# Optimization experiments

Hardware: AMD Instinct MI355X
Metric: run time of the kernel (lower is better)

## Reference

```python
import jax, jax.numpy as jnp
import numpy as np

N_NODES = 50000
N_EDGES = 800000
N_GRAPHS = 256
IN_DIM, HIDDEN_DIM, EMBED_DIM = 128, 64, 128


def setup_inputs() -> dict:
    key = jax.random.key(0)
    ks = jax.random.split(key, 8)
    x = jax.random.normal(ks[0], (N_NODES, IN_DIM), dtype=jnp.float32)
    edge_index = jax.random.randint(ks[1], (2, N_EDGES), 0, N_NODES, dtype=jnp.int64)
    edge_weight = jax.random.uniform(ks[2], (N_EDGES,), dtype=jnp.float32)
    batch_vec = jnp.sort(jax.random.randint(ks[3], (N_NODES,), 0, N_GRAPHS, dtype=jnp.int64))
    # Glorot-ish params for the two GCNConv layers
    W1 = jax.random.normal(ks[4], (IN_DIM, HIDDEN_DIM), dtype=jnp.float32) / np.sqrt(IN_DIM)
    b1 = jnp.zeros((HIDDEN_DIM,), dtype=jnp.float32)
    W2 = jax.random.normal(ks[5], (HIDDEN_DIM, EMBED_DIM), dtype=jnp.float32) / np.sqrt(HIDDEN_DIM)
    b2 = jnp.zeros((EMBED_DIM,), dtype=jnp.float32)
    return {"x": x, "edge_index": edge_index, "edge_weight": edge_weight,
            "batch_vec": batch_vec, "W1": W1, "b1": b1, "W2": W2, "b2": b2}


def _gcn_conv(x, src, dst, ew, W, b, num_nodes):
    # PyG GCNConv: linear transform, add self-loops (weight 1), sym-normalize, aggregate at dst.
    h = x @ W  # [N, out]
    loops = jnp.arange(num_nodes, dtype=src.dtype)
    row = jnp.concatenate([src, loops])
    col = jnp.concatenate([dst, loops])
    w = jnp.concatenate([ew, jnp.ones((num_nodes,), x.dtype)])
    deg = jax.ops.segment_sum(w, col, num_segments=num_nodes)
    dis = jnp.where(deg > 0, jax.lax.rsqrt(deg), 0.0)  # deg^{-1/2}, inf -> 0
    norm = dis[row] * w * dis[col]  # [E+N]
    msg = h[row] * norm[:, None]  # gather + scale
    out = jax.ops.segment_sum(msg, col, num_segments=num_nodes)  # scatter-add
    return out + b


def reference(x, edge_index, edge_weight, batch_vec, W1, b1, W2, b2):
    src, dst = edge_index[0], edge_index[1]
    h = jax.nn.relu(_gcn_conv(x, src, dst, edge_weight, W1, b1, N_NODES))
    # dropout is identity at inference
    h = jax.nn.relu(_gcn_conv(h, src, dst, edge_weight, W2, b2, N_NODES))
    # global_mean_pool over graphs
    s = jax.ops.segment_sum(h, batch_vec, num_segments=N_GRAPHS)
    cnt = jax.ops.segment_sum(jnp.ones((N_NODES,), h.dtype), batch_vec, num_segments=N_GRAPHS)
    return s / jnp.maximum(cnt, 1.0)[:, None]
```

## Files before the change

### kernel.cpp

```cpp
#include <hip/hip_runtime.h>

constexpr int N_NODES  = 50000;
constexpr int N_EDGES  = 800000;
constexpr int N_GRAPHS = 256;
constexpr int IN_DIM   = 128;
constexpr int HID      = 64;
constexpr int EMB      = 128;
constexpr int NBKT     = 391;
constexpr int BCAP     = 4096;
constexpr int EB       = (N_EDGES + 1023) / 1024;
constexpr int GB       = (N_NODES + 31) / 32;
constexpr int GSB      = (N_NODES + 255) / 256;
constexpr int NB2      = 64;

constexpr size_t OFF_POOL = 0;
constexpr size_t OFF_GCUR = 32768;
constexpr size_t OFF_GST  = 33160;
constexpr size_t OFF_DIS  = 33424;
constexpr size_t OFF_RS   = 83424;
constexpr size_t OFF_REC  = 133424;
constexpr size_t OFF_PART = OFF_REC + 2 * (size_t)NBKT * BCAP;
constexpr size_t OFF_H1   = OFF_PART;
constexpr size_t OFF_H1P  = OFF_PART + 4 * (size_t)NBKT * BCAP;
constexpr size_t OFF_AGG2 = OFF_H1P;

__device__ inline unsigned bf16r(float f) {
    unsigned u = __float_as_uint(f);
    return (u + 0x7fffu + ((u >> 16) & 1u)) >> 16;
}
__device__ inline unsigned bf16pack2(float lo, float hi) {
    return bf16r(lo) | (bf16r(hi) << 16);
}
__device__ inline float bflo(unsigned v) { return __uint_as_float(v << 16); }
__device__ inline float bfhi(unsigned v) { return __uint_as_float(v & 0xffff0000u); }

__device__ inline void fma4(float4& acc, float s, const float4& v) {
    acc.x += s * v.x; acc.y += s * v.y; acc.z += s * v.z; acc.w += s * v.w;
}

__global__ __launch_bounds__(256) void k_p2(const int* __restrict__ src,
                                            const int* __restrict__ dst,
                                            const float* __restrict__ ew,
                                            int* __restrict__ gcur,
                                            uint4* __restrict__ part,
                                            const int* __restrict__ batch,
                                            int* __restrict__ gstart) {
    __shared__ int   lb[NBKT];
    __shared__ int   lc[NBKT];
    __shared__ int   es[1024];
    __shared__ int   ed[1024];
    __shared__ float ee[1024];
    int tid = threadIdx.x;
    if (blockIdx.x >= EB) {
        int i = (blockIdx.x - EB) * 256 + tid;
        if (i >= N_NODES) return;
        int g = batch[i];
        if (i == 0) {
            for (int gg = 0; gg <= g; ++gg) gstart[gg] = 0;
        } else {
            int gp = batch[i - 1];
            for (int gg = gp + 1; gg <= g; ++gg) gstart[gg] = i;
        }
        if (i == N_NODES - 1) {
            for (int gg = g + 1; gg <= N_GRAPHS; ++gg) gstart[gg] = N_NODES;
        }
        return;
    }
    for (int i = tid; i < NBKT; i += 256) lc[i] = 0;
    __syncthreads();
    int base = blockIdx.x * 1024;
    #pragma unroll
    for (int j = 0; j < 4; ++j) {
        int idx = j * 256 + tid;
        int e = base + idx;
        int d = 0, s = 0; float w = 0.f;
        if (e < N_EDGES) {
            d = dst[e]; s = src[e]; w = ew[e];
            atomicAdd(&lc[d >> 7], 1);
        }
        es[idx] = s; ed[idx] = d; ee[idx] = w;
    }
    __syncthreads();
    for (int i = tid; i < NBKT; i += 256) {
        int c = lc[i];
        lb[i] = c ? (i * BCAP + atomicAdd(&gcur[i], c)) : 0;
        lc[i] = 0;
    }
    __syncthreads();
    #pragma unroll
    for (int j = 0; j < 4; ++j) {
        int idx = j * 256 + tid;
        int e = base + idx;
        if (e < N_EDGES) {
            int d = ed[idx];
            int b = d >> 7;
            int r = atomicAdd(&lc[b], 1);
            part[lb[b] + r] = make_uint4((unsigned)es[idx], (unsigned)d,
                                         __float_as_uint(ee[idx]), 0u);
        }
    }
}

constexpr int SMEM_BYTES = 32768 + 32 * (IN_DIM + 4) * 4;
__global__ __launch_bounds__(256) void k_p3_gemm1(const uint4* __restrict__ part,
                                                  const int* __restrict__ gcur,
                                                  int* __restrict__ rs,
                                                  float* __restrict__ dis,
                                                  uint2* __restrict__ rec,
                                                  const float* __restrict__ x,
                                                  const float* __restrict__ W1,
                                                  unsigned* __restrict__ h) {
    __shared__ alignas(16) unsigned char smem[SMEM_BYTES];
    int tid = threadIdx.x;
    if (blockIdx.x < NBKT) {
        uint2* cache = (uint2*)smem;
        int*   cnt   = (int*)(smem + 32768);
        float* dgw   = (float*)(smem + 32768 + 512);
        int*   scn   = (int*)(smem + 32768 + 1024);
        int*   curx  = (int*)(smem + 32768 + 1536);
        int b = blockIdx.x;
        int ebeg = b * BCAP;
        int ne = gcur[b]; if (ne > BCAP) ne = BCAP;
        if (tid < 128) { cnt[tid] = 0; dgw[tid] = 0.f; }
        __syncthreads();
        for (int i = tid; i < ne; i += 256) {
            uint4 r = part[ebeg + i];
            int ld = (int)r.y & 127;
            cache[i] = make_uint2(r.x | ((unsigned)ld << 16), r.z);
            atomicAdd(&cnt[ld], 1);
            atomicAdd(&dgw[ld], __uint_as_float(r.z));
        }
        __syncthreads();
        int c  = (tid < 128) ? cnt[tid] : 0;
        int pc = (c + 1) & ~1;
        if (tid < 128) scn[tid] = pc;
        __syncthreads();
        for (int off = 1; off < 128; off <<= 1) {
            int a = (tid >= off && tid < 128) ? scn[tid - off] : 0;
            __syncthreads();
            if (tid < 128) scn[tid] += a;
            __syncthreads();
        }
        if (tid < 128) {
            int start = ebeg + scn[tid] - pc;
            int node = (b << 7) + tid;
            if (node < N_NODES) {
                rs[node] = start + c;
                dis[node] = rsqrtf(dgw[tid] + 1.0f);
            }
            curx[tid] = start;
        }
        __syncthreads();
        for (int i = tid; i < ne; i += 256) {
            uint2 q = cache[i];
            int ld = (int)(q.x >> 16);
            int pos = atomicAdd(&curx[ld], 1);
            rec[pos] = make_uint2(q.x & 0xFFFFu, q.y);
        }
        return;
    }
    float* Ws = (float*)smem;
    float (*xs)[IN_DIM + 4] = (float (*)[IN_DIM + 4])(smem + 32768);
    int bid = blockIdx.x - NBKT;
    const float4* W4 = (const float4*)W1;
    float4* Ws4 = (float4*)Ws;
    for (int i = tid; i < IN_DIM * HID / 4; i += 256) Ws4[i] = W4[i];
    int base = bid * 32;
    const float4* X4 = (const float4*)x;
    for (int i = tid; i < 32 * 32; i += 256) {
        int ln = i >> 5, kq = i & 31;
        int node = base + ln;
        float4 v = (node < N_NODES) ? X4[(size_t)node * 32 + kq]
                                    : make_float4(0.f, 0.f, 0.f, 0.f);
        *(float4*)&xs[ln][kq * 4] = v;
    }
    __syncthreads();
    int np = tid >> 4;
    int q  = tid & 15;
    int n0 = np * 2, n1 = n0 + 1;
    float4 a0 = make_float4(0.f, 0.f, 0.f, 0.f);
    float4 a1 = a0;
    #pragma unroll 4
    for (int k4 = 0; k4 < IN_DIM; k4 += 4) {
        float4 xv0 = *(const float4*)&xs[n0][k4];
        float4 xv1 = *(const float4*)&xs[n1][k4];
        float4 w0 = Ws4[(k4 + 0) * 16 + q];
        float4 w1 = Ws4[(k4 + 1) * 16 + q];
        float4 w2 = Ws4[(k4 + 2) * 16 + q];
        float4 w3 = Ws4[(k4 + 3) * 16 + q];
        fma4(a0, xv0.x, w0); fma4(a0, xv0.y, w1); fma4(a0, xv0.z, w2); fma4(a0, xv0.w, w3);
        fma4(a1, xv1.x, w0); fma4(a1, xv1.y, w1); fma4(a1, xv1.z, w2); fma4(a1, xv1.w, w3);
    }
    int nd0 = base + n0, nd1 = base + n1;
    if (nd0 < N_NODES) {
        uint2 p = make_uint2(bf16pack2(a0.x, a0.y), bf16pack2(a0.z, a0.w));
        ((uint2*)h)[(size_t)nd0 * 16 + q] = p;
    }
    if (nd1 < N_NODES) {
        uint2 p = make_uint2(bf16pack2(a1.x, a1.y), bf16pack2(a1.z, a1.w));
        ((uint2*)h)[(size_t)nd1 * 16 + q] = p;
    }
}

template <bool PASS1>
__global__ __launch_bounds__(256) void k_gather64(unsigned* __restrict__ recw,
                                                  const int* __restrict__ rs,
                                                  const float* __restrict__ dis,
                                                  const unsigned* __restrict__ T,
                                                  const float* __restrict__ bias,
                                                  void* __restrict__ outv) {
    int wave = (blockIdx.x * 256 + threadIdx.x) >> 6;
    if (wave >= N_NODES) return;
    int lane = threadIdx.x & 63;
    int grp  = lane >> 4;
    int l    = lane & 15;
    int n = wave;
    int begin = ((n & 127) == 0) ? ((n >> 7) * BCAP) : ((rs[n - 1] + 1) & ~1);
    int end = rs[n];
    const uint2* T2 = (const uint2*)T;
    const uint4* R4 = (const uint4*)recw;

    float a0 = 0.f, a1 = 0.f, a2 = 0.f, a3 = 0.f;
    float c0 = 0.f, c1 = 0.f, c2 = 0.f, c3 = 0.f;
    for (int k = begin + 2 * grp; k < end; k += 8) {
        uint4 q = R4[k >> 1];
        unsigned s0 = q.x;
        float w0;
        if (PASS1) {
            w0 = dis[s0] * __uint_as_float(q.y);
            if (l == 0) recw[2 * k + 1] = __float_as_uint(w0);
        } else {
            w0 = __uint_as_float(q.y);
        }
        uint2 t0 = T2[(size_t)s0 * 16 + l];
        a0 += bflo(t0.x) * w0; a1 += bfhi(t0.x) * w0;
        a2 += bflo(t0.y) * w0; a3 += bfhi(t0.y) * w0;
        if (k + 1 < end) {
            unsigned s1 = q.z;
            float w1;
            if (PASS1) {
                w1 = dis[s1] * __uint_as_float(q.w);
                if (l == 0) recw[2 * k + 3] = __float_as_uint(w1);
            } else {
                w1 = __uint_as_float(q.w);
            }
            uint2 t1 = T2[(size_t)s1 * 16 + l];
            c0 += bflo(t1.x) * w1; c1 += bfhi(t1.x) * w1;
            c2 += bflo(t1.y) * w1; c3 += bfhi(t1.y) * w1;
        }
    }
    a0 += c0; a1 += c1; a2 += c2; a3 += c3;
    a0 += __shfl_xor(a0, 16, 64); a1 += __shfl_xor(a1, 16, 64);
    a2 += __shfl_xor(a2, 16, 64); a3 += __shfl_xor(a3, 16, 64);
    a0 += __shfl_xor(a0, 32, 64); a1 += __shfl_xor(a1, 32, 64);
    a2 += __shfl_xor(a2, 32, 64); a3 += __shfl_xor(a3, 32, 64);
    if (grp == 0) {
        float di = dis[n];
        uint2 t = T2[(size_t)n * 16 + l];
        a0 += bflo(t.x) * di; a1 += bfhi(t.x) * di;
        a2 += bflo(t.y) * di; a3 += bfhi(t.y) * di;
        a0 *= di; a1 *= di; a2 *= di; a3 *= di;
        if (PASS1) {
            float4 b = ((const float4*)bias)[l];
            a0 = fmaxf(a0 + b.x, 0.f);
            a1 = fmaxf(a1 + b.y, 0.f);
            a2 = fmaxf(a2 + b.z, 0.f);
            a3 = fmaxf(a3 + b.w, 0.f);
            ((uint2*)outv)[(size_t)n * 16 + l] =
                make_uint2(bf16pack2(a0, a1), bf16pack2(a2, a3));
        } else {
            ((float4*)outv)[(size_t)n * 16 + l] = make_float4(a0, a1, a2, a3);
        }
    }
}

__global__ __launch_bounds__(256) void k_gemm2_pool(const float* __restrict__ agg,
                                                    const float* __restrict__ W2,
                                                    const float* __restrict__ b2,
                                                    const int* __restrict__ batch,
                                                    float* __restrict__ pool) {
    __shared__ float Ws[HID * EMB];
    __shared__ float as[NB2][HID];
    __shared__ int   bs[NB2];
    int tid = threadIdx.x;
    const float4* W4 = (const float4*)W2;
    float4* Ws4 = (float4*)Ws;
    for (int i = tid; i < HID * EMB / 4; i += 256) Ws4[i] = W4[i];
    int base = blockIdx.x * NB2;
    const float4* A4 = (const float4*)agg;
    float4* as4 = (float4*)as;
    for (int i = tid; i < NB2 * HID / 4; i += 256) {
        int node = base + (i >> 4);
        as4[i] = (node < N_NODES) ? A4[(size_t)node * 16 + (i & 15)]
                                  : make_float4(0.f, 0.f, 0.f, 0.f);
    }
    if (tid < NB2) {
        int node = base + tid;
        bs[tid] = (node < N_NODES) ? batch[node] : -1;
    }
    __syncthreads();

    int c = tid & 31;
    int s = tid >> 5;
    int jc = c * 4;
    int nb = s * 8;
    float4 acc[8];
    #pragma unroll
    for (int i = 0; i < 8; ++i) acc[i] = make_float4(0.f, 0.f, 0.f, 0.f);
    #pragma unroll 4
    for (int k4 = 0; k4 < HID; k4 += 4) {
        float4 w0 = Ws4[(k4 + 0) * 32 + c];
        float4 w1 = Ws4[(k4 + 1) * 32 + c];
        float4 w2 = Ws4[(k4 + 2) * 32 + c];
        float4 w3 = Ws4[(k4 + 3) * 32 + c];
        #pragma unroll
        for (int i = 0; i < 8; ++i) {
            float4 av = *(const float4*)&as[nb + i][k4];
            fma4(acc[i], av.x, w0); fma4(acc[i], av.y, w1);
            fma4(acc[i], av.z, w2); fma4(acc[i], av.w, w3);
        }
    }
    float4 bq = *(const float4*)&b2[jc];
    float4 racc = make_float4(0.f, 0.f, 0.f, 0.f);
    int gcur = -1;
    #pragma unroll
    for (int i = 0; i < 8; ++i) {
        int g = bs[nb + i];
        if (g != gcur) {
            if (gcur >= 0) {
                float* p = &pool[(size_t)gcur * EMB + jc];
                atomicAdd(p + 0, racc.x); atomicAdd(p + 1, racc.y);
                atomicAdd(p + 2, racc.z); atomicAdd(p + 3, racc.w);
            }
            racc = make_float4(0.f, 0.f, 0.f, 0.f);
            gcur = g;
        }
        if (g < 0) continue;
        racc.x += fmaxf(acc[i].x + bq.x, 0.f);
        racc.y += fmaxf(acc[i].y + bq.y, 0.f);
        racc.z += fmaxf(acc[i].z + bq.z, 0.f);
        racc.w += fmaxf(acc[i].w + bq.w, 0.f);
    }
    if (gcur >= 0) {
        float* p = &pool[(size_t)gcur * EMB + jc];
        atomicAdd(p + 0, racc.x); atomicAdd(p + 1, racc.y);
        atomicAdd(p + 2, racc.z); atomicAdd(p + 3, racc.w);
    }
}

__global__ void k_divide(const float* __restrict__ pool, const int* __restrict__ gstart,
                         float* __restrict__ out) {
    int idx = blockIdx.x * blockDim.x + threadIdx.x;
    if (idx >= N_GRAPHS * EMB) return;
    int g = idx >> 7;
    float c = (float)(gstart[g + 1] - gstart[g]);
    out[idx] = pool[idx] / fmaxf(c, 1.0f);
}

extern "C" void kernel_launch(void* const* d_in, const int* in_sizes, int n_in,
                              void* d_out, int out_size, void* d_ws, size_t ws_size,
                              hipStream_t stream) {
    const float* x     = (const float*)d_in[0];
    const int*   eidx  = (const int*)d_in[1];
    const float* ew    = (const float*)d_in[2];
    const int*   batch = (const int*)d_in[3];
    const float* W1    = (const float*)d_in[4];
    const float* b1    = (const float*)d_in[5];
    const float* W2    = (const float*)d_in[6];
    const float* b2    = (const float*)d_in[7];
    float* out = (float*)d_out;

    const int* src = eidx;
    const int* dst = eidx + N_EDGES;

    float* ws     = (float*)d_ws;
    float* pool   = ws + OFF_POOL;
    int*   gcur   = (int*)(ws + OFF_GCUR);
    int*   gstart = (int*)(ws + OFF_GST);
    float* dis    = ws + OFF_DIS;
    int*   rs     = (int*)(ws + OFF_RS);
    uint2* rec    = (uint2*)(ws + OFF_REC);
    uint4* part   = (uint4*)(ws + OFF_PART);
    unsigned* h1  = (unsigned*)(ws + OFF_H1);
    unsigned* h1p = (unsigned*)(ws + OFF_H1P);
    float* agg2   = ws + OFF_AGG2;

    (void)hipMemsetAsync(pool, 0, (size_t)(32768 + NBKT) * sizeof(float), stream);

    k_p2<<<EB + GSB, 256, 0, stream>>>(src, dst, ew, gcur, part, batch, gstart);

    k_p3_gemm1<<<NBKT + GB, 256, 0, stream>>>(part, gcur, rs, dis, rec, x, W1, h1p);

    k_gather64<true><<<N_NODES / 4, 256, 0, stream>>>((unsigned*)rec, rs, dis, h1p, b1, h1);

    k_gather64<false><<<N_NODES / 4, 256, 0, stream>>>((unsigned*)rec, rs, dis, h1, nullptr, agg2);

    k_gemm2_pool<<<(N_NODES + NB2 - 1) / NB2, 256, 0, stream>>>(agg2, W2, b2, batch, pool);

    k_divide<<<(N_GRAPHS * EMB + 255) / 256, 256, 0, stream>>>(pool, gstart, out);
}
```

Measured before the change: 235.2 us.

## Replace per-node CSR gather with per-bucket LDS-atomic aggregation

Removes the in-bucket counting sort, prefix scan and record rewrite that built a per-destination CSR. Degree is now computed directly from the bucketed edge records. Each aggregation pass assigns one block per 128-node bucket and accumulates messages into a shared-memory tile with float atomics, then adds the self-loop, normalisation, bias and ReLU. This saves a preprocessing phase and its global traffic. The cost is only 391 blocks instead of one wave per node, a serial loop over about 2K edges per block, LDS atomic contention, and recomputing dis[src]*w in both passes.

Measured after the change: 858.6 us. 3.65x slower.

```diff
diff --git a/kernel.cpp b/kernel.cpp
--- a/kernel.cpp
+++ b/kernel.cpp
@@ -17,11 +17,9 @@
 constexpr size_t OFF_GCUR = 32768;
 constexpr size_t OFF_GST  = 33160;
 constexpr size_t OFF_DIS  = 33424;
-constexpr size_t OFF_RS   = 83424;
-constexpr size_t OFF_REC  = 133424;
-constexpr size_t OFF_PART = OFF_REC + 2 * (size_t)NBKT * BCAP;
-constexpr size_t OFF_H1   = OFF_PART;
-constexpr size_t OFF_H1P  = OFF_PART + 4 * (size_t)NBKT * BCAP;
+constexpr size_t OFF_PART = 83424;
+constexpr size_t OFF_H1   = OFF_PART + 4 * (size_t)NBKT * BCAP;
+constexpr size_t OFF_H1P  = OFF_H1 + 2 * (size_t)N_NODES * 16;
 constexpr size_t OFF_AGG2 = OFF_H1P;
 
 __device__ inline unsigned bf16r(float f) {
@@ -102,60 +100,29 @@
 }
 
 constexpr int SMEM_BYTES = 32768 + 32 * (IN_DIM + 4) * 4;
-__global__ __launch_bounds__(256) void k_p3_gemm1(const uint4* __restrict__ part,
-                                                  const int* __restrict__ gcur,
-                                                  int* __restrict__ rs,
-                                                  float* __restrict__ dis,
-                                                  uint2* __restrict__ rec,
-                                                  const float* __restrict__ x,
-                                                  const float* __restrict__ W1,
-                                                  unsigned* __restrict__ h) {
+__global__ __launch_bounds__(256) void k_dis_gemm1(const uint4* __restrict__ part,
+                                                   const int* __restrict__ gcur,
+                                                   float* __restrict__ dis,
+                                                   const float* __restrict__ x,
+                                                   const float* __restrict__ W1,
+                                                   unsigned* __restrict__ h) {
     __shared__ alignas(16) unsigned char smem[SMEM_BYTES];
     int tid = threadIdx.x;
     if (blockIdx.x < NBKT) {
-        uint2* cache = (uint2*)smem;
-        int*   cnt   = (int*)(smem + 32768);
-        float* dgw   = (float*)(smem + 32768 + 512);
-        int*   scn   = (int*)(smem + 32768 + 1024);
-        int*   curx  = (int*)(smem + 32768 + 1536);
+        float* dgw = (float*)smem;
+        if (tid < 128) dgw[tid] = 0.f;
+        __syncthreads();
         int b = blockIdx.x;
         int ebeg = b * BCAP;
         int ne = gcur[b]; if (ne > BCAP) ne = BCAP;
-        if (tid < 128) { cnt[tid] = 0; dgw[tid] = 0.f; }
-        __syncthreads();
         for (int i = tid; i < ne; i += 256) {
             uint4 r = part[ebeg + i];
-            int ld = (int)r.y & 127;
-            cache[i] = make_uint2(r.x | ((unsigned)ld << 16), r.z);
-            atomicAdd(&cnt[ld], 1);
-            atomicAdd(&dgw[ld], __uint_as_float(r.z));
+            atomicAdd(&dgw[(int)r.y & 127], __uint_as_float(r.z));
         }
         __syncthreads();
-        int c  = (tid < 128) ? cnt[tid] : 0;
-        int pc = (c + 1) & ~1;
-        if (tid < 128) scn[tid] = pc;
-        __syncthreads();
-        for (int off = 1; off < 128; off <<= 1) {
-            int a = (tid >= off && tid < 128) ? scn[tid - off] : 0;
-            __syncthreads();
-            if (tid < 128) scn[tid] += a;
-            __syncthreads();
-        }
         if (tid < 128) {
-            int start = ebeg + scn[tid] - pc;
             int node = (b << 7) + tid;
-            if (node < N_NODES) {
-                rs[node] = start + c;
-                dis[node] = rsqrtf(dgw[tid] + 1.0f);
-            }
-            curx[tid] = start;
-        }
-        __syncthreads();
-        for (int i = tid; i < ne; i += 256) {
-            uint2 q = cache[i];
-            int ld = (int)(q.x >> 16);
-            int pos = atomicAdd(&curx[ld], 1);
-            rec[pos] = make_uint2(q.x & 0xFFFFu, q.y);
+            if (node < N_NODES) dis[node] = rsqrtf(dgw[tid] + 1.0f);
         }
         return;
     }
@@ -203,73 +170,60 @@
 }
 
 template <bool PASS1>
-__global__ __launch_bounds__(256) void k_gather64(unsigned* __restrict__ recw,
-                                                  const int* __restrict__ rs,
-                                                  const float* __restrict__ dis,
-                                                  const unsigned* __restrict__ T,
-                                                  const float* __restrict__ bias,
-                                                  void* __restrict__ outv) {
-    int wave = (blockIdx.x * 256 + threadIdx.x) >> 6;
-    if (wave >= N_NODES) return;
-    int lane = threadIdx.x & 63;
-    int grp  = lane >> 4;
-    int l    = lane & 15;
-    int n = wave;
-    int begin = ((n & 127) == 0) ? ((n >> 7) * BCAP) : ((rs[n - 1] + 1) & ~1);
-    int end = rs[n];
+__global__ __launch_bounds__(256) void k_gatherB(const uint4* __restrict__ part,
+                                                 const int* __restrict__ gcur,
+                                                 const float* __restrict__ dis,
+                                                 const unsigned* __restrict__ T,
+                                                 const float* __restrict__ bias,
+                                                 void* __restrict__ outv) {
+    __shared__ float acc[128][65];
+    int tid = threadIdx.x;
+    for (int i = tid; i < 128 * 65; i += 256) ((float*)acc)[i] = 0.f;
+    __syncthreads();
+    int b = blockIdx.x;
+    int ebeg = b * BCAP;
+    int ne = gcur[b]; if (ne > BCAP) ne = BCAP;
+    int l  = tid & 15;
+    int eg = tid >> 4;
     const uint2* T2 = (const uint2*)T;
-    const uint4* R4 = (const uint4*)recw;
-
-    float a0 = 0.f, a1 = 0.f, a2 = 0.f, a3 = 0.f;
-    float c0 = 0.f, c1 = 0.f, c2 = 0.f, c3 = 0.f;
-    for (int k = begin + 2 * grp; k < end; k += 8) {
-        uint4 q = R4[k >> 1];
-        unsigned s0 = q.x;
-        float w0;
-        if (PASS1) {
-            w0 = dis[s0] * __uint_as_float(q.y);
-            if (l == 0) recw[2 * k + 1] = __float_as_uint(w0);
-        } else {
-            w0 = __uint_as_float(q.y);
-        }
-        uint2 t0 = T2[(size_t)s0 * 16 + l];
-        a0 += bflo(t0.x) * w0; a1 += bfhi(t0.x) * w0;
-        a2 += bflo(t0.y) * w0; a3 += bfhi(t0.y) * w0;
-        if (k + 1 < end) {
-            unsigned s1 = q.z;
-            float w1;
-            if (PASS1) {
-                w1 = dis[s1] * __uint_as_float(q.w);
-                if (l == 0) recw[2 * k + 3] = __float_as_uint(w1);
-            } else {
-                w1 = __uint_as_float(q.w);
-            }
-            uint2 t1 = T2[(size_t)s1 * 16 + l];
-            c0 += bflo(t1.x) * w1; c1 += bfhi(t1.x) * w1;
-            c2 += bflo(t1.y) * w1; c3 += bfhi(t1.y) * w1;
-        }
-    }
-    a0 += c0; a1 += c1; a2 += c2; a3 += c3;
-    a0 += __shfl_xor(a0, 16, 64); a1 += __shfl_xor(a1, 16, 64);
-    a2 += __shfl_xor(a2, 16, 64); a3 += __shfl_xor(a3, 16, 64);
-    a0 += __shfl_xor(a0, 32, 64); a1 += __shfl_xor(a1, 32, 64);
-    a2 += __shfl_xor(a2, 32, 64); a3 += __shfl_xor(a3, 32, 64);
-    if (grp == 0) {
+    for (int i0 = 0; i0 < ne; i0 += 16) {
+        int e = i0 + eg;
+        if (e < ne) {
+            uint4 r = part[ebeg + e];
+            unsigned s = r.x;
+            int ld = (int)r.y & 127;
+            float w = dis[s] * __uint_as_float(r.z);
+            uint2 t = T2[(size_t)s * 16 + l];
+            float* a = &acc[ld][4 * l];
+            atomicAdd(a + 0, bflo(t.x) * w);
+            atomicAdd(a + 1, bfhi(t.x) * w);
+            atomicAdd(a + 2, bflo(t.y) * w);
+            atomicAdd(a + 3, bfhi(t.y) * w);
+        }
+    }
+    __syncthreads();
+    int base_node = b << 7;
+    for (int it = tid; it < 128 * 16; it += 256) {
+        int ln = it >> 4, q = it & 15;
+        int n = base_node + ln;
+        if (n >= N_NODES) continue;
         float di = dis[n];
-        uint2 t = T2[(size_t)n * 16 + l];
-        a0 += bflo(t.x) * di; a1 += bfhi(t.x) * di;
-        a2 += bflo(t.y) * di; a3 += bfhi(t.y) * di;
+        uint2 t = T2[(size_t)n * 16 + q];
+        float a0 = acc[ln][4 * q + 0] + bflo(t.x) * di;
+        float a1 = acc[ln][4 * q + 1] + bfhi(t.x) * di;
+        float a2 = acc[ln][4 * q + 2] + bflo(t.y) * di;
+        float a3 = acc[ln][4 * q + 3] + bfhi(t.y) * di;
         a0 *= di; a1 *= di; a2 *= di; a3 *= di;
         if (PASS1) {
-            float4 b = ((const float4*)bias)[l];
-            a0 = fmaxf(a0 + b.x, 0.f);
-            a1 = fmaxf(a1 + b.y, 0.f);
-            a2 = fmaxf(a2 + b.z, 0.f);
-            a3 = fmaxf(a3 + b.w, 0.f);
-            ((uint2*)outv)[(size_t)n * 16 + l] =
+            float4 bq = ((const float4*)bias)[q];
+            a0 = fmaxf(a0 + bq.x, 0.f);
+            a1 = fmaxf(a1 + bq.y, 0.f);
+            a2 = fmaxf(a2 + bq.z, 0.f);
+            a3 = fmaxf(a3 + bq.w, 0.f);
+            ((uint2*)outv)[(size_t)n * 16 + q] =
                 make_uint2(bf16pack2(a0, a1), bf16pack2(a2, a3));
         } else {
-            ((float4*)outv)[(size_t)n * 16 + l] = make_float4(a0, a1, a2, a3);
+            ((float4*)outv)[(size_t)n * 16 + q] = make_float4(a0, a1, a2, a3);
         }
     }
 }
@@ -378,8 +332,6 @@
     int*   gcur   = (int*)(ws + OFF_GCUR);
     int*   gstart = (int*)(ws + OFF_GST);
     float* dis    = ws + OFF_DIS;
-    int*   rs     = (int*)(ws + OFF_RS);
-    uint2* rec    = (uint2*)(ws + OFF_REC);
     uint4* part   = (uint4*)(ws + OFF_PART);
     unsigned* h1  = (unsigned*)(ws + OFF_H1);
     unsigned* h1p = (unsigned*)(ws + OFF_H1P);
@@ -389,11 +341,11 @@
 
     k_p2<<<EB + GSB, 256, 0, stream>>>(src, dst, ew, gcur, part, batch, gstart);
 
-    k_p3_gemm1<<<NBKT + GB, 256, 0, stream>>>(part, gcur, rs, dis, rec, x, W1, h1p);
-
-    k_gather64<true><<<N_NODES / 4, 256, 0, stream>>>((unsigned*)rec, rs, dis, h1p, b1, h1);
-
-    k_gather64<false><<<N_NODES / 4, 256, 0, stream>>>((unsigned*)rec, rs, dis, h1, nullptr, agg2);
+    k_dis_gemm1<<<NBKT + GB, 256, 0, stream>>>(part, gcur, dis, x, W1, h1p);
+
+    k_gatherB<true><<<NBKT, 256, 0, stream>>>(part, gcur, dis, h1p, b1, h1);
+
+    k_gatherB<false><<<NBKT, 256, 0, stream>>>(part, gcur, dis, h1, nullptr, agg2);
 
     k_gemm2_pool<<<(N_NODES + NB2 - 1) / NB2, 256, 0, stream>>>(agg2, W2, b2, batch, pool);
 
```
